# Performance work log

Measured on AMD Instinct MI355X. Metric: run time of the kernel, lower is better.

Reference implementation:

```python
import jax, jax.numpy as jnp
import numpy as np

D = 256          # d_embed
KD = 256         # key_d_embed
NHEAD = 8
DK = D // NHEAD  # 32
QH = QW = 128
QWS = 16
KH = KW = 64
KWS = 8
R = QWS // KWS   # qk_ratio = 2
SCALE = 1.0 / np.sqrt(DK)


def _rel_index():
    # query coords on fine grid, key coords scaled up by ratio R
    qc = np.stack(np.meshgrid(np.arange(QWS), np.arange(QWS), indexing='ij'), -1).reshape(-1, 2)
    kc = np.stack(np.meshgrid(np.arange(KWS), np.arange(KWS), indexing='ij'), -1).reshape(-1, 2) * R
    rel = qc[:, None, :] - kc[None, :, :] + (QWS - R)  # values in [0, 2*QWS-R-1]
    return jnp.asarray(rel[..., 0] * (2 * QWS - R) + rel[..., 1])  # (QWS^2, KWS^2)


def _partition(t, ws):
    # (B, h, H, W, d) -> (B, h, H/ws, W/ws, ws*ws, d)
    B, h, H, W, d = t.shape
    t = t.reshape(B, h, H // ws, ws, W // ws, ws, d).transpose(0, 1, 2, 4, 3, 5, 6)
    return t.reshape(B, h, H // ws, W // ws, ws * ws, d)


def _merge(t, ws, H, W):
    # inverse of _partition
    B, h, nH, nW, _, d = t.shape
    t = t.reshape(B, h, nH, nW, ws, ws, d).transpose(0, 1, 2, 4, 3, 5, 6)
    return t.reshape(B, h, H, W, d)


def setup_inputs() -> dict:
    key = jax.random.key(0)
    ks = jax.random.split(key, 9)
    x = jax.random.normal(ks[0], (8, QH, QW, D), dtype=jnp.float32)
    z = jax.random.normal(ks[1], (8, KH, KW, KD), dtype=jnp.float32)
    mask = jax.random.randint(ks[2], (1, NHEAD, QH // QWS, QW // QWS, QWS * QWS, KWS * KWS), 0, 2) == 1
    Wq = jax.random.normal(ks[3], (D, D), dtype=jnp.float32) * 0.02
    bq = jnp.zeros((D,), dtype=jnp.float32)
    Wkv = jax.random.normal(ks[4], (KD, 2 * D), dtype=jnp.float32) * 0.02
    bkv = jnp.zeros((2 * D,), dtype=jnp.float32)
    Wo = jax.random.normal(ks[5], (D, D), dtype=jnp.float32) * 0.02
    bo = jnp.zeros((D,), dtype=jnp.float32)
    rel_table = jax.random.normal(ks[6], ((2 * QWS - R) ** 2, NHEAD), dtype=jnp.float32) * 0.02
    return {"x": x, "z": z, "mask": mask, "Wq": Wq, "bq": bq, "Wkv": Wkv, "bkv": bkv, "Wo": Wo, "bo": bo, "rel_table": rel_table}


def reference(x, z, mask, Wq, bq, Wkv, bkv, Wo, bo, rel_table):
    B, H, W, _ = x.shape
    q = (x @ Wq + bq).reshape(B, H, W, NHEAD, DK).transpose(0, 3, 1, 2, 4)        # (B,h,H,W,dk)
    kv = (z @ Wkv + bkv).reshape(B, KH, KW, 2, NHEAD, DK).transpose(3, 0, 4, 1, 2, 5)
    k, v = kv[0], kv[1]                                                           # (B,h,_H,_W,dk)
    sq, sk = QWS // 2, KWS // 2
    q = jnp.roll(q, (-sq, -sq), axis=(2, 3))
    k = jnp.roll(k, (-sk, -sk), axis=(2, 3))
    v = jnp.roll(v, (-sk, -sk), axis=(2, 3))
    q = _partition(q, QWS)   # (B,h,nh,nw,QWS^2,dk)
    k = _partition(k, KWS)   # (B,h,nh,nw,KWS^2,dk)
    v = _partition(v, KWS)
    attn = jnp.einsum('bhnmqd,bhnmkd->bhnmqk', q, k) * SCALE
    bias = rel_table[_rel_index()].transpose(2, 0, 1)[None, :, None, None]        # (1,h,1,1,QWS^2,KWS^2)
    attn = attn + bias
    attn = jnp.where(mask, jnp.float32(-1e9), attn)
    attn = jax.nn.softmax(attn, axis=-1)
    out = jnp.einsum('bhnmqk,bhnmkd->bhnmqd', attn, v)
    out = _merge(out, QWS, H, W)
    out = jnp.roll(out, (sq, sq), axis=(2, 3))
    out = out.transpose(0, 2, 3, 1, 4).reshape(B, H, W, D)
    return out @ Wo + bo
```

## Files before the change

kernel.cpp:

```cpp
#include <hip/hip_runtime.h>
#include <hip/hip_bf16.h>
#include <type_traits>


typedef __attribute__((ext_vector_type(8))) short short8v;
typedef __attribute__((ext_vector_type(4))) float f32x4;
typedef __attribute__((ext_vector_type(8))) unsigned short ushort8v;
typedef unsigned long long u64;

#define DEV __device__ __forceinline__

DEV unsigned short f2bf(float f) {
    union { float f; unsigned u; } v; v.f = f;
    unsigned r = v.u + 0x7FFFu + ((v.u >> 16) & 1u);
    return (unsigned short)(r >> 16);
}

DEV short8v cvt_f32x8(const float4 lo, const float4 hi) {
    union U { __hip_bfloat162 h[4]; short8v s; } u;
    u.h[0] = __float22bfloat162_rn(float2{lo.x, lo.y});
    u.h[1] = __float22bfloat162_rn(float2{lo.z, lo.w});
    u.h[2] = __float22bfloat162_rn(float2{hi.x, hi.y});
    u.h[3] = __float22bfloat162_rn(float2{hi.z, hi.w});
    return u.s;
}

DEV uint2 pack4(f32x4 v) {
    union { __hip_bfloat162 h; unsigned u; } a, b;
    a.h = __float22bfloat162_rn(float2{v[0], v[1]});
    b.h = __float22bfloat162_rn(float2{v[2], v[3]});
    return uint2{a.u, b.u};
}

#define ATT_SCALE 0.17677669529663687f

__global__ void prep_weights(const float* __restrict__ Wq, const float* __restrict__ Wkv,
                             const float* __restrict__ Wo,
                             unsigned short* __restrict__ WqT, unsigned short* __restrict__ WkvT,
                             unsigned short* __restrict__ WoT) {
    int idx = blockIdx.x * 256 + threadIdx.x;
    if (idx < 65536) {
        int n = idx >> 8, k = idx & 255;
        WqT[idx] = f2bf(Wq[k * 256 + n] * ATT_SCALE);
    } else if (idx < 196608) {
        int i = idx - 65536;
        int n = i >> 8, k = i & 255;
        WkvT[i] = f2bf(Wkv[k * 512 + n]);
    } else {
        int i = idx - 196608;
        int n = i >> 8, k = i & 255;
        WoT[i] = f2bf(Wo[k * 256 + n]);
    }
}

__global__ void prep_bias(const float* __restrict__ rel_table, const float* __restrict__ bq,
                          float* __restrict__ biasb, float* __restrict__ bqs) {
    int idx = blockIdx.x * 256 + threadIdx.x;
    if (idx < 131072) {
        int head = idx >> 14;
        int q = (idx >> 6) & 255;
        int k = idx & 63;
        int qi = q >> 4, qj = q & 15;
        int ki = k >> 3, kj = k & 7;
        int r0 = qi - 2 * ki + 14, r1 = qj - 2 * kj + 14;
        biasb[idx] = rel_table[(r0 * 30 + r1) * 8 + head];
    } else if (idx < 131328) {
        int i = idx - 131072;
        bqs[i] = bq[i] * ATT_SCALE;
    }
}

__global__ void prep_mask(const int* __restrict__ mask, u64* __restrict__ mp) {
    int idx = blockIdx.x * 256 + threadIdx.x;
    const int4* src = reinterpret_cast<const int4*>(mask + (size_t)idx * 64);
    u64 bits = 0;
#pragma unroll
    for (int c = 0; c < 16; ++c) {
        int4 v = src[c];
        if (v.x) bits |= 1ull << (c * 4 + 0);
        if (v.y) bits |= 1ull << (c * 4 + 1);
        if (v.z) bits |= 1ull << (c * 4 + 2);
        if (v.w) bits |= 1ull << (c * 4 + 3);
    }
    mp[idx] = bits;
}

template <bool AF32, bool OUT_BF16>
__global__ __launch_bounds__(512, 2) void gemm_ws(
    const void* __restrict__ Ain, const unsigned short* __restrict__ BT,
    const float* __restrict__ bias, void* __restrict__ Cout)
{
    __shared__ __align__(16) unsigned char Wl[131072];
    const float* Af = (const float*)Ain;
    const unsigned short* Ab = (const unsigned short*)Ain;

    const int tid = threadIdx.x;
    const int w = tid >> 6, lane = tid & 63, lr = lane & 15, lg = lane >> 4;
    const size_t wm = (size_t)blockIdx.x * 512 + w * 64;

    {
        int r = tid >> 1, half = tid & 1;
        const unsigned short* src = BT + r * 256 + half * 128;
        int rsw = (r >> 1) & 3;
#pragma unroll
        for (int kk = 0; kk < 4; ++kk) {
            int kt = half * 4 + kk;
#pragma unroll
            for (int sl = 0; sl < 4; ++sl) {
                ushort8v v = *reinterpret_cast<const ushort8v*>(src + kk * 32 + sl * 8);
                *reinterpret_cast<ushort8v*>(
                    &Wl[kt * 16384 + r * 64 + ((sl ^ rsw) << 4)]) = v;
            }
        }
    }
    __syncthreads();

    const int swzb = (lg ^ ((lr >> 1) & 3)) << 4;
    const int colb = lg * 4;

#define RD_W(kt, nt) (*reinterpret_cast<const short8v*>( \
        &Wl[(kt) * 16384 + ((nt) * 16 + lr) * 64 + swzb]))

#define EPILOGUE(t)                                                             \
    _Pragma("unroll")                                                           \
    for (int nt = 0; nt < 16; ++nt) {                                           \
        f32x4 b4 = *reinterpret_cast<const f32x4*>(bias + nt * 16 + colb);      \
        f32x4 v = acc[nt] + b4;                                                 \
        size_t row = wm + (t) * 16 + lr;                                        \
        if constexpr (OUT_BF16)                                                 \
            *reinterpret_cast<uint2*>(                                          \
                (unsigned short*)Cout + row * 256 + nt * 16 + colb) = pack4(v); \
        else                                                                    \
            *reinterpret_cast<f32x4*>(                                          \
                (float*)Cout + row * 256 + nt * 16 + colb) = v;                 \
    }

    if constexpr (AF32) {
        float4 bufA[16], bufB[16];
#define LOADT_F(BUF, t) {                                                       \
        const float* p = Af + (wm + (t) * 16 + lr) * 256 + lg * 8;              \
        _Pragma("unroll")                                                       \
        for (int kt = 0; kt < 8; ++kt) {                                        \
            BUF[kt * 2]     = *reinterpret_cast<const float4*>(p + kt * 32);    \
            BUF[kt * 2 + 1] = *reinterpret_cast<const float4*>(p + kt * 32 + 4);\
        } }
#define COMP_F(BUF, t) {                                                        \
        f32x4 acc[16];                                                          \
        _Pragma("unroll")                                                       \
        for (int nt = 0; nt < 16; ++nt) acc[nt] = {0.f, 0.f, 0.f, 0.f};         \
        _Pragma("unroll")                                                       \
        for (int kt = 0; kt < 8; ++kt) {                                        \
            short8v a = cvt_f32x8(BUF[kt * 2], BUF[kt * 2 + 1]);                \
            _Pragma("unroll")                                                   \
            for (int nt = 0; nt < 16; ++nt)                                     \
                acc[nt] = __builtin_amdgcn_mfma_f32_16x16x32_bf16(              \
                    RD_W(kt, nt), a, acc[nt], 0, 0, 0);                         \
        }                                                                       \
        EPILOGUE(t) }
        LOADT_F(bufA, 0);
        LOADT_F(bufB, 1); COMP_F(bufA, 0);
        LOADT_F(bufA, 2); COMP_F(bufB, 1);
        LOADT_F(bufB, 3); COMP_F(bufA, 2);
        COMP_F(bufB, 3);
#undef LOADT_F
#undef COMP_F
    } else {
        short8v bufA[8], bufB[8], bufC[8];
#define LOADT_B(BUF, t) {                                                       \
        const unsigned short* p = Ab + (wm + (t) * 16 + lr) * 256 + lg * 8;     \
        _Pragma("unroll")                                                       \
        for (int kt = 0; kt < 8; ++kt)                                          \
            BUF[kt] = *reinterpret_cast<const short8v*>(p + kt * 32); }
#define COMP_B(BUF, t) {                                                        \
        f32x4 acc[16];                                                          \
        _Pragma("unroll")                                                       \
        for (int nt = 0; nt < 16; ++nt) acc[nt] = {0.f, 0.f, 0.f, 0.f};         \
        _Pragma("unroll")                                                       \
        for (int kt = 0; kt < 8; ++kt) {                                        \
            _Pragma("unroll")                                                   \
            for (int nt = 0; nt < 16; ++nt)                                     \
                acc[nt] = __builtin_amdgcn_mfma_f32_16x16x32_bf16(              \
                    RD_W(kt, nt), BUF[kt], acc[nt], 0, 0, 0);                   \
        }                                                                       \
        EPILOGUE(t) }
        LOADT_B(bufA, 0); LOADT_B(bufB, 1); LOADT_B(bufC, 2);
        COMP_B(bufA, 0); LOADT_B(bufA, 3);
        COMP_B(bufB, 1);
        COMP_B(bufC, 2);
        COMP_B(bufA, 3);
#undef LOADT_B
#undef COMP_B
    }
#undef RD_W
#undef EPILOGUE
}

template <bool AF32, bool OUT_BF16>
__global__ __launch_bounds__(256) void gemm_proj(
    const void* __restrict__ Ain, const unsigned short* __restrict__ BT,
    const float* __restrict__ bias, void* __restrict__ Cout,
    int M, int N, int K)
{
    __shared__ __align__(16) unsigned char As[2][8192];
    __shared__ __align__(16) unsigned char Bs[2][8192];
    const float* Af = (const float*)Ain;

    const int tid = threadIdx.x;
    const int mb = blockIdx.y * 128, nb = blockIdx.x * 128;
    const int w = tid >> 6, lane = tid & 63, lr = lane & 15, lg = lane >> 4;
    const int wm = (w >> 1) * 64, wn = (w & 1) * 64;

    const int cr0 = (w << 5) + (lane >> 2);
    const int csp = lane & 3;
    const int cs0 = csp ^ ((cr0 >> 1) & 3);
    const int cs1 = csp ^ (((cr0 + 16) >> 1) & 3);

    auto stageB = [&](int buf, int kb) {
        __builtin_amdgcn_global_load_lds(
            (const __attribute__((address_space(1))) void*)(BT + (size_t)(nb + cr0) * K + kb + cs0 * 8),
            (__attribute__((address_space(3))) void*)(&Bs[buf][w << 11]), 16, 0, 0);
        __builtin_amdgcn_global_load_lds(
            (const __attribute__((address_space(1))) void*)(BT + (size_t)(nb + cr0 + 16) * K + kb + cs1 * 8),
            (__attribute__((address_space(3))) void*)(&Bs[buf][(w << 11) + 1024]), 16, 0, 0);
    };

    float4 areg[2][2];
    auto loadA = [&](int kb) {
#pragma unroll
        for (int i = 0; i < 2; ++i) {
            int flat = tid + (i << 8);
            int r = flat >> 2, sp = flat & 3;
            int s = sp ^ ((r >> 1) & 3);
            const float* src = Af + (size_t)(mb + r) * K + kb + s * 8;
            areg[i][0] = *reinterpret_cast<const float4*>(src);
            areg[i][1] = *reinterpret_cast<const float4*>(src + 4);
        }
    };
    auto writeA = [&](int buf) {
#pragma unroll
        for (int i = 0; i < 2; ++i) {
            int flat = tid + (i << 8);
            int r = flat >> 2, sp = flat & 3;
            ushort8v u = { f2bf(areg[i][0].x), f2bf(areg[i][0].y),
                           f2bf(areg[i][0].z), f2bf(areg[i][0].w),
                           f2bf(areg[i][1].x), f2bf(areg[i][1].y),
                           f2bf(areg[i][1].z), f2bf(areg[i][1].w) };
            *reinterpret_cast<ushort8v*>(&As[buf][r * 64 + sp * 16]) = u;
        }
    };
    auto rdA = [&](int buf, int row) -> short8v {
        int swz = (lg ^ ((row >> 1) & 3)) << 4;
        return *reinterpret_cast<const short8v*>(&As[buf][row * 64 + swz]);
    };
    auto rdB = [&](int buf, int row) -> short8v {
        int swz = (lg ^ ((row >> 1) & 3)) << 4;
        return *reinterpret_cast<const short8v*>(&Bs[buf][row * 64 + swz]);
    };

    f32x4 acc[4][4];
#pragma unroll
    for (int i = 0; i < 4; ++i)
#pragma unroll
        for (int j = 0; j < 4; ++j) acc[i][j] = {0.f, 0.f, 0.f, 0.f};

    loadA(0); stageB(0, 0); writeA(0);
    __syncthreads();

    const int NT = K >> 5;
    int cur = 0;
    for (int t = 0; t < NT; ++t) {
        if (t + 1 < NT) { loadA((t + 1) << 5); stageB(cur ^ 1, (t + 1) << 5); }
        short8v af[4], bfr[4];
#pragma unroll
        for (int mt = 0; mt < 4; ++mt) af[mt] = rdA(cur, wm + mt * 16 + lr);
#pragma unroll
        for (int nt = 0; nt < 4; ++nt) bfr[nt] = rdB(cur, wn + nt * 16 + lr);
#pragma unroll
        for (int mt = 0; mt < 4; ++mt)
#pragma unroll
            for (int nt = 0; nt < 4; ++nt)
                acc[mt][nt] = __builtin_amdgcn_mfma_f32_16x16x32_bf16(
                    af[mt], bfr[nt], acc[mt][nt], 0, 0, 0);
        if (t + 1 < NT) writeA(cur ^ 1);
        __syncthreads();
        cur ^= 1;
    }

#pragma unroll
    for (int mt = 0; mt < 4; ++mt)
#pragma unroll
        for (int nt = 0; nt < 4; ++nt)
#pragma unroll
            for (int j = 0; j < 4; ++j) {
                int row = mb + wm + mt * 16 + lg * 4 + j;
                int col = nb + wn + nt * 16 + lr;
                float v = acc[mt][nt][j] + bias[col];
                if constexpr (OUT_BF16)
                    ((unsigned short*)Cout)[(size_t)row * N + col] = f2bf(v);
                else
                    ((float*)Cout)[(size_t)row * N + col] = v;
            }
}

__global__ __launch_bounds__(256) void win_attn(
    unsigned short* __restrict__ Qbuf,
    const unsigned short* __restrict__ KVbuf,
    const u64* __restrict__ maskp,
    const float* __restrict__ biasb)
{
    __shared__ __align__(16) unsigned char Pb[256 * 128];
    __shared__ __align__(16) unsigned short Vt[32][72];

    const int tid = threadIdx.x;
    const int win = blockIdx.x, head = blockIdx.y, b = blockIdx.z;
    const int wi = win >> 3, wj = win & 7;
    const int w = tid >> 6, lane = tid & 63, lr = lane & 15, lg = lane >> 4;
    const int qb = w * 64;

    {
        int key = tid & 63, c = tid >> 6;
        int kr = (wi * 8 + (key >> 3) + 4) & 63;
        int kc = (wj * 8 + (key & 7) + 4) & 63;
        ushort8v v = *reinterpret_cast<const ushort8v*>(
            KVbuf + ((size_t)(b * 4096 + kr * 64 + kc)) * 512 + 256 + head * 32 + c * 8);
#pragma unroll
        for (int e = 0; e < 8; ++e) Vt[c * 8 + e][key] = v[e];
    }

    short8v qf[4], kf[4];
#pragma unroll
    for (int mt = 0; mt < 4; ++mt) {
        int q = qb + mt * 16 + lr;
        int gr = (wi * 16 + (q >> 4) + 8) & 127;
        int gc = (wj * 16 + (q & 15) + 8) & 127;
        qf[mt] = *reinterpret_cast<const short8v*>(
            Qbuf + ((size_t)(b * 16384 + gr * 128 + gc)) * 256 + head * 32 + lg * 8);
    }
#pragma unroll
    for (int nt = 0; nt < 4; ++nt) {
        int key = nt * 16 + lr;
        int kr = (wi * 8 + (key >> 3) + 4) & 63;
        int kc = (wj * 8 + (key & 7) + 4) & 63;
        kf[nt] = *reinterpret_cast<const short8v*>(
            KVbuf + ((size_t)(b * 4096 + kr * 64 + kc)) * 512 + head * 32 + lg * 8);
    }

    f32x4 s[4][4];
#pragma unroll
    for (int mt = 0; mt < 4; ++mt)
#pragma unroll
        for (int nt = 0; nt < 4; ++nt) s[mt][nt] = {0.f, 0.f, 0.f, 0.f};
    __builtin_amdgcn_s_setprio(1);
#pragma unroll
    for (int mt = 0; mt < 4; ++mt)
#pragma unroll
        for (int nt = 0; nt < 4; ++nt)
            s[mt][nt] = __builtin_amdgcn_mfma_f32_16x16x32_bf16(qf[mt], kf[nt], s[mt][nt], 0, 0, 0);
    __builtin_amdgcn_s_setprio(0);

    const u64* mrow = maskp + (size_t)(head * 64 + win) * 256;
#pragma unroll
    for (int mt = 0; mt < 4; ++mt) {
#pragma unroll
        for (int j = 0; j < 4; ++j) {
            int q = qb + mt * 16 + lg * 4 + j;
            u64 mb = mrow[q];
            const float* brow = biasb + (size_t)(head * 256 + q) * 64;
            float v[4];
            float m = -3.0e38f;
#pragma unroll
            for (int nt = 0; nt < 4; ++nt) {
                int key = nt * 16 + lr;
                float sv = s[mt][nt][j] + brow[key];
                if ((mb >> key) & 1ull) sv = -1.0e9f;
                v[nt] = sv;
                m = fmaxf(m, sv);
            }
#pragma unroll
            for (int d = 1; d < 16; d <<= 1) m = fmaxf(m, __shfl_xor(m, d, 64));
            float sum = 0.f;
#pragma unroll
            for (int nt = 0; nt < 4; ++nt) { v[nt] = __expf(v[nt] - m); sum += v[nt]; }
#pragma unroll
            for (int d = 1; d < 16; d <<= 1) sum += __shfl_xor(sum, d, 64);
            float inv = 1.0f / sum;
            int sw = (q & 7) << 4;
#pragma unroll
            for (int nt = 0; nt < 4; ++nt) {
                int off = q * 128 + (((nt * 16 + lr) * 2) ^ sw);
                *reinterpret_cast<unsigned short*>(Pb + off) = f2bf(v[nt] * inv);
            }
        }
    }

    __syncthreads();

    f32x4 o[4][2];
#pragma unroll
    for (int mt = 0; mt < 4; ++mt)
#pragma unroll
        for (int nt = 0; nt < 2; ++nt) o[mt][nt] = {0.f, 0.f, 0.f, 0.f};
#pragma unroll
    for (int kc = 0; kc < 2; ++kc) {
        short8v pf[4], vf[2];
#pragma unroll
        for (int mt = 0; mt < 4; ++mt) {
            int row = qb + mt * 16 + lr;
            int coff = (kc * 64 + lg * 16) ^ ((row & 7) << 4);
            pf[mt] = *reinterpret_cast<const short8v*>(Pb + row * 128 + coff);
        }
#pragma unroll
        for (int nt = 0; nt < 2; ++nt)
            vf[nt] = *reinterpret_cast<const short8v*>(&Vt[nt * 16 + lr][kc * 32 + lg * 8]);
        __builtin_amdgcn_s_setprio(1);
#pragma unroll
        for (int mt = 0; mt < 4; ++mt)
#pragma unroll
            for (int nt = 0; nt < 2; ++nt)
                o[mt][nt] = __builtin_amdgcn_mfma_f32_16x16x32_bf16(pf[mt], vf[nt], o[mt][nt], 0, 0, 0);
        __builtin_amdgcn_s_setprio(0);
    }

#pragma unroll
    for (int mt = 0; mt < 4; ++mt)
#pragma unroll
        for (int j = 0; j < 4; ++j) {
            int q = qb + mt * 16 + lg * 4 + j;
            int gr = (wi * 16 + (q >> 4) + 8) & 127;
            int gc = (wj * 16 + (q & 15) + 8) & 127;
            unsigned short* dst =
                Qbuf + ((size_t)(b * 16384 + gr * 128 + gc)) * 256 + head * 32;
#pragma unroll
            for (int nt = 0; nt < 2; ++nt)
                dst[nt * 16 + lr] = f2bf(o[mt][nt][j]);
        }
}

extern "C" void kernel_launch(void* const* d_in, const int* in_sizes, int n_in,
                              void* d_out, int out_size, void* d_ws, size_t ws_size,
                              hipStream_t stream) {
    const float* x    = (const float*)d_in[0];
    const float* z    = (const float*)d_in[1];
    const int*   mask = (const int*)d_in[2];
    const float* Wq   = (const float*)d_in[3];
    const float* bq   = (const float*)d_in[4];
    const float* Wkv  = (const float*)d_in[5];
    const float* bkv  = (const float*)d_in[6];
    const float* Wo   = (const float*)d_in[7];
    const float* bo   = (const float*)d_in[8];
    const float* rel  = (const float*)d_in[9];
    float* out = (float*)d_out;

    char* ws = (char*)d_ws;
    unsigned short* Qbuf  = (unsigned short*)(ws);
    unsigned short* KVbuf = (unsigned short*)(ws + 67108864);
    unsigned short* WqT   = (unsigned short*)(ws + 100663296);
    unsigned short* WkvT  = (unsigned short*)(ws + 100794368);
    unsigned short* WoT   = (unsigned short*)(ws + 101056512);
    float*          biasb = (float*)(ws + 101187584);
    u64*            maskp = (u64*)(ws + 101711872);
    float*          bqs   = (float*)(ws + 102760448);

    prep_weights<<<1024, 256, 0, stream>>>(Wq, Wkv, Wo, WqT, WkvT, WoT);
    prep_bias<<<513, 256, 0, stream>>>(rel, bq, biasb, bqs);
    prep_mask<<<512, 256, 0, stream>>>(mask, maskp);

    gemm_ws<true, true><<<256, 512, 0, stream>>>(
        (const void*)x, WqT, bqs, (void*)Qbuf);
    gemm_proj<true, true><<<dim3(4, 256), 256, 0, stream>>>(
        (const void*)z, WkvT, bkv, (void*)KVbuf, 32768, 512, 256);
    win_attn<<<dim3(64, 8, 8), 256, 0, stream>>>(Qbuf, KVbuf, maskp, biasb);
    gemm_ws<false, false><<<256, 512, 0, stream>>>(
        (const void*)Qbuf, WoT, bo, (void*)out);
}
```

Measured before the change: 225.1 us.

## Use register-resident weights with LDS-ring async A loads for output projection

```diff
diff --git a/kernel.cpp b/kernel.cpp
--- a/kernel.cpp
+++ b/kernel.cpp
@@ -85,6 +85,83 @@
     mp[idx] = bits;
 }
 
+__global__ __launch_bounds__(512, 2) void gemm_rs(
+    const unsigned short* __restrict__ A,
+    const unsigned short* __restrict__ WT,
+    const float* __restrict__ bias, float* __restrict__ out)
+{
+    __shared__ __align__(16) unsigned char R[131072];
+
+    const int tid = threadIdx.x;
+    const int w = tid >> 6, lane = tid & 63, lr = lane & 15, lg = lane >> 4;
+    const int g = w >> 2, wn = (w & 3) * 64;
+    const size_t rowbase = (size_t)blockIdx.x * 512 + (size_t)g * 256;
+
+    short8v wf[8][4];
+#pragma unroll
+    for (int kt = 0; kt < 8; ++kt)
+#pragma unroll
+        for (int nt = 0; nt < 4; ++nt)
+            wf[kt][nt] = *reinterpret_cast<const short8v*>(
+                WT + (size_t)(wn + nt * 16 + lr) * 256 + kt * 32 + lg * 8);
+
+    const int r_ = lane >> 5;
+    const int u_ = lane & 31;
+    unsigned char* ringbase = R + w * 16384;
+    const unsigned char* Ab = (const unsigned char*)A;
+
+    auto issue = [&](int t, int slot) {
+        size_t gbyte0 = (rowbase + (size_t)t * 16) * 512;
+        unsigned char* ldst = ringbase + slot * 8192;
+#pragma unroll
+        for (int c = 0; c < 8; ++c) {
+            int r = 2 * c + r_;
+            int v = u_ ^ r;
+            __builtin_amdgcn_global_load_lds(
+                (const __attribute__((address_space(1))) void*)
+                    (Ab + gbyte0 + (size_t)r * 512 + v * 16),
+                (__attribute__((address_space(3))) void*)(ldst + c * 1024),
+                16, 0, 0);
+        }
+    };
+
+    issue(0, 0);
+
+    for (int t = 0; t < 16; ++t) {
+        const int slot = t & 1;
+        if (t == 0) asm volatile("s_waitcnt vmcnt(0)" ::: "memory");
+        else        asm volatile("s_waitcnt vmcnt(4)" ::: "memory");
+        __builtin_amdgcn_sched_barrier(0);
+
+        short8v af[8];
+#pragma unroll
+        for (int kt = 0; kt < 8; ++kt)
+            af[kt] = *reinterpret_cast<const short8v*>(
+                ringbase + slot * 8192 + lr * 512 + (((kt * 4 + lg) ^ lr) << 4));
+        __builtin_amdgcn_sched_barrier(0);
+
+        if (t + 1 < 16) issue(t + 1, slot ^ 1);
+
+        f32x4 acc[4];
+#pragma unroll
+        for (int nt = 0; nt < 4; ++nt) acc[nt] = {0.f, 0.f, 0.f, 0.f};
+#pragma unroll
+        for (int kt = 0; kt < 8; ++kt)
+#pragma unroll
+            for (int nt = 0; nt < 4; ++nt)
+                acc[nt] = __builtin_amdgcn_mfma_f32_16x16x32_bf16(
+                    wf[kt][nt], af[kt], acc[nt], 0, 0, 0);
+
+        size_t row = rowbase + (size_t)t * 16 + lr;
+#pragma unroll
+        for (int nt = 0; nt < 4; ++nt) {
+            f32x4 b4 = *reinterpret_cast<const f32x4*>(bias + wn + nt * 16 + lg * 4);
+            *reinterpret_cast<f32x4*>(out + row * 256 + wn + nt * 16 + lg * 4)
+                = acc[nt] + b4;
+        }
+    }
+}
+
 template <bool AF32, bool OUT_BF16>
 __global__ __launch_bounds__(512, 2) void gemm_ws(
     const void* __restrict__ Ain, const unsigned short* __restrict__ BT,
@@ -92,7 +169,6 @@
 {
     __shared__ __align__(16) unsigned char Wl[131072];
     const float* Af = (const float*)Ain;
-    const unsigned short* Ab = (const unsigned short*)Ain;
 
     const int tid = threadIdx.x;
     const int w = tid >> 6, lane = tid & 63, lr = lane & 15, lg = lane >> 4;
@@ -135,8 +211,7 @@
                 (float*)Cout + row * 256 + nt * 16 + colb) = v;                 \
     }
 
-    if constexpr (AF32) {
-        float4 bufA[16], bufB[16];
+    float4 bufA[16], bufB[16];
 #define LOADT_F(BUF, t) {                                                       \
         const float* p = Af + (wm + (t) * 16 + lr) * 256 + lg * 8;              \
         _Pragma("unroll")                                                       \
@@ -157,40 +232,13 @@
                     RD_W(kt, nt), a, acc[nt], 0, 0, 0);                         \
         }                                                                       \
         EPILOGUE(t) }
-        LOADT_F(bufA, 0);
-        LOADT_F(bufB, 1); COMP_F(bufA, 0);
-        LOADT_F(bufA, 2); COMP_F(bufB, 1);
-        LOADT_F(bufB, 3); COMP_F(bufA, 2);
-        COMP_F(bufB, 3);
+    LOADT_F(bufA, 0);
+    LOADT_F(bufB, 1); COMP_F(bufA, 0);
+    LOADT_F(bufA, 2); COMP_F(bufB, 1);
+    LOADT_F(bufB, 3); COMP_F(bufA, 2);
+    COMP_F(bufB, 3);
 #undef LOADT_F
 #undef COMP_F
-    } else {
-        short8v bufA[8], bufB[8], bufC[8];
-#define LOADT_B(BUF, t) {                                                       \
-        const unsigned short* p = Ab + (wm + (t) * 16 + lr) * 256 + lg * 8;     \
-        _Pragma("unroll")                                                       \
-        for (int kt = 0; kt < 8; ++kt)                                          \
-            BUF[kt] = *reinterpret_cast<const short8v*>(p + kt * 32); }
-#define COMP_B(BUF, t) {                                                        \
-        f32x4 acc[16];                                                          \
-        _Pragma("unroll")                                                       \
-        for (int nt = 0; nt < 16; ++nt) acc[nt] = {0.f, 0.f, 0.f, 0.f};         \
-        _Pragma("unroll")                                                       \
-        for (int kt = 0; kt < 8; ++kt) {                                        \
-            _Pragma("unroll")                                                   \
-            for (int nt = 0; nt < 16; ++nt)                                     \
-                acc[nt] = __builtin_amdgcn_mfma_f32_16x16x32_bf16(              \
-                    RD_W(kt, nt), BUF[kt], acc[nt], 0, 0, 0);                   \
-        }                                                                       \
-        EPILOGUE(t) }
-        LOADT_B(bufA, 0); LOADT_B(bufB, 1); LOADT_B(bufC, 2);
-        COMP_B(bufA, 0); LOADT_B(bufA, 3);
-        COMP_B(bufB, 1);
-        COMP_B(bufC, 2);
-        COMP_B(bufA, 3);
-#undef LOADT_B
-#undef COMP_B
-    }
 #undef RD_W
 #undef EPILOGUE
 }
@@ -470,6 +518,5 @@
     gemm_proj<true, true><<<dim3(4, 256), 256, 0, stream>>>(
         (const void*)z, WkvT, bkv, (void*)KVbuf, 32768, 512, 256);
     win_attn<<<dim3(64, 8, 8), 256, 0, stream>>>(Qbuf, KVbuf, maskp, biasb);
-    gemm_ws<false, false><<<256, 512, 0, stream>>>(
-        (const void*)Qbuf, WoT, bo, (void*)out);
-}
+    gemm_rs<<<256, 512, 0, stream>>>(Qbuf, WoT, bo, out);
+}
```

After: 219.2 us. -2.6%, faster.
